# Kernel optimization log

Measured on AMD Instinct MI355X. Metric: run time of the kernel, lower is better.

Reference implementation:

```python
import jax, jax.numpy as jnp
import numpy as np

N, P, C, H, W, M = 2, 3, 80, 64, 64, 524288
HID = 64
BOX_WARP = 2.0


def _linear_init(key, fan_in, fan_out):
    # kaiming-uniform-ish; bias is zero-init per the torch module
    bound = 1.0 / np.sqrt(fan_in)
    return jax.random.uniform(key, (fan_in, fan_out), jnp.float32, -bound, bound)


def setup_inputs() -> dict:
    key = jax.random.key(0)
    ks = jax.random.split(key, 6)
    planes = jax.random.normal(ks[0], (N, P, C, H, W), jnp.float32)
    coordinates = jax.random.uniform(ks[1], (N, M, 3), jnp.float32, -1.0, 1.0)
    W1 = _linear_init(ks[2], 3 * C, HID)
    W2 = _linear_init(ks[3], HID, HID)
    W3 = _linear_init(ks[4], HID, HID)
    W4 = _linear_init(ks[5], HID, 1)
    return {
        "planes": planes, "coordinates": coordinates,
        "W1": W1, "b1": jnp.zeros((HID,), jnp.float32),
        "W2": W2, "b2": jnp.zeros((HID,), jnp.float32),
        "W3": W3, "b3": jnp.zeros((HID,), jnp.float32),
        "W4": W4, "b4": jnp.zeros((1,), jnp.float32),
    }


def _grid_sample_bilinear(feat, grid):
    # feat: [B, C, H, W]; grid: [B, M, 2] in [-1, 1] (x, y order),
    # bilinear, padding_mode='zeros', align_corners=False (matches torch).
    B, Cc, Hh, Ww = feat.shape
    gx = (grid[..., 0] + 1.0) * (Ww * 0.5) - 0.5  # [B, M]
    gy = (grid[..., 1] + 1.0) * (Hh * 0.5) - 0.5
    x0 = jnp.floor(gx)
    y0 = jnp.floor(gy)
    wx1 = gx - x0
    wy1 = gy - y0
    featf = feat.transpose(0, 2, 3, 1).reshape(B, Hh * Ww, Cc)  # [B, HW, C]

    def gather(xi, yi):
        valid = (xi >= 0) & (xi < Ww) & (yi >= 0) & (yi < Hh)
        xc = jnp.clip(xi, 0, Ww - 1).astype(jnp.int32)
        yc = jnp.clip(yi, 0, Hh - 1).astype(jnp.int32)
        idx = yc * Ww + xc  # [B, M]
        v = jnp.take_along_axis(featf, idx[..., None], axis=1)  # [B, M, C]
        return v * valid[..., None].astype(feat.dtype)

    v00 = gather(x0, y0)
    v01 = gather(x0 + 1, y0)
    v10 = gather(x0, y0 + 1)
    v11 = gather(x0 + 1, y0 + 1)
    wx1 = wx1[..., None]
    wy1 = wy1[..., None]
    top = v00 * (1.0 - wx1) + v01 * wx1
    bot = v10 * (1.0 - wx1) + v11 * wx1
    return top * (1.0 - wy1) + bot * wy1  # [B, M, C]


def _plane_axes():
    return jnp.array(
        [[[1, 0, 0], [0, 1, 0], [0, 0, 1]],
         [[1, 0, 0], [0, 0, 1], [0, 1, 0]],
         [[0, 0, 1], [0, 1, 0], [1, 0, 0]]], jnp.float32)


def reference(planes, coordinates, W1, b1, W2, b2, W3, b3, W4, b4):
    n, p, c, h, w = planes.shape
    m = coordinates.shape[1]
    inv_axes = jnp.linalg.inv(_plane_axes())  # [3, 3, 3]
    coords = (2.0 / BOX_WARP) * coordinates  # [N, M, 3]
    # project: coords @ inv_plane per plane, keep first two coords
    proj = jnp.einsum('nmc,pcd->npmd', coords, inv_axes)[..., :2]  # [N, P, M, 2]
    feat = planes.reshape(n * p, c, h, w)
    grid = proj.reshape(n * p, m, 2)
    samp = _grid_sample_bilinear(feat, grid)  # [N*P, M, C]
    # [N, P, M, C] -> [N, M, P*C]
    x = samp.reshape(n, p, m, c).transpose(0, 2, 1, 3).reshape(n, m, p * c)
    hdn = jax.nn.relu(x @ W1 + b1)
    hdn = jax.nn.relu(hdn @ W2 + b2)
    hdn = jax.nn.relu(hdn @ W3 + b3)
    sdf = hdn @ W4 + b4  # [N, M, 1]
    return sdf
```

## Files before the change

### kernel.cpp

```cpp
#include <hip/hip_runtime.h>
#include <hip/hip_bf16.h>
#include <stdint.h>

#define MPTS  524288
#define NB    2
#define CCH   80
#define HWDIM 64
#define HID   64
#define NPTS  (NB * MPTS)

typedef _Float16 f16x2 __attribute__((ext_vector_type(2)));
typedef _Float16 f16x8 __attribute__((ext_vector_type(8)));
typedef float    f32x4 __attribute__((ext_vector_type(4)));

union FragH { uint4 q; f16x8 v; f16x2 h2[4]; _Float16 h[8]; };

__device__ __forceinline__ void fma_mix_lo(float& acc, unsigned u, float w) {
    asm volatile("v_fma_mix_f32 %0, %1, %2, %0 op_sel_hi:[1,0,0]"
                 : "+v"(acc) : "v"(u), "v"(w));
}
__device__ __forceinline__ void fma_mix_hi(float& acc, unsigned u, float w) {
    asm volatile("v_fma_mix_f32 %0, %1, %2, %0 op_sel:[1,0,0] op_sel_hi:[1,0,0]"
                 : "+v"(acc) : "v"(u), "v"(w));
}

__global__ void precompute_planesW(const float* __restrict__ planes,
                                   const float* __restrict__ W1,
                                   unsigned short* __restrict__ planesW) {
    __shared__ float tA[CCH * 64];
    __shared__ float tW[CCH * 64];
    int b  = blockIdx.x;
    int np = b >> 6, y = b & 63;
    int p  = np % 3;
    int t  = threadIdx.x;
    for (int i = t; i < CCH * 64; i += 256) {
        int c = i >> 6, x = i & 63;
        tA[i] = planes[((size_t)np * CCH + c) * 4096 + y * 64 + x];
        tW[i] = W1[(p * CCH + c) * HID + x];
    }
    __syncthreads();
    int px = t >> 2;
    int n0 = (t & 3) * 16;
    float acc[16];
    #pragma unroll
    for (int i = 0; i < 16; ++i) acc[i] = 0.0f;
    for (int c = 0; c < CCH; ++c) {
        float a = tA[c * 64 + px];
        #pragma unroll
        for (int i = 0; i < 16; ++i) acc[i] += a * tW[c * 64 + n0 + i];
    }
    unsigned short* dst = planesW + (((size_t)np * 4096) + y * 64 + px) * HID + n0;
    #pragma unroll
    for (int i = 0; i < 16; ++i) {
        union { _Float16 h; unsigned short u; } cv;
        cv.h = (_Float16)acc[i];
        dst[i] = cv.u;
    }
}

__global__ void pack_weights23(const float* __restrict__ W2,
                               const float* __restrict__ W3,
                               unsigned short* __restrict__ wpack) {
    int e = blockIdx.x * 256 + threadIdx.x;
    const float* W = (e < 4096) ? W2 : W3;
    int q  = e & 4095;
    int j  = q & 7;
    int l  = (q >> 3) & 63;
    int nt = (q >> 9) & 3;
    int kb = q >> 11;
    int k  = kb * 32 + ((l >> 4) << 3) + j;
    int nn = nt * 16 + (l & 15);
    union { _Float16 h; unsigned short u; } cv;
    cv.h = (_Float16)W[k * HID + nn];
    wpack[e] = cv.u;
}

__global__ __launch_bounds__(256, 4) void fused_kernel(
        const unsigned short* __restrict__ planesW,
        const float* __restrict__ coords,
        const unsigned short* __restrict__ wpack,
        const float* __restrict__ b1, const float* __restrict__ b2,
        const float* __restrict__ b3, const float* __restrict__ W4,
        const float* __restrict__ b4, float* __restrict__ out) {

    __shared__ __align__(16) unsigned short sH[4 * 16 * 72];
    __shared__ __align__(16) uint4 sSet[64][3][2];
    __shared__ __align__(16) unsigned short sW23[8192];
    __shared__ float sBias[196];

    int t    = threadIdx.x;
    int wave = t >> 6, lane = t & 63;
    int ptbase = blockIdx.x * 64 + wave * 16;

    unsigned short* hw = sH + wave * (16 * 72);
    _Float16* hwh = (_Float16*)hw;

    {
        const uint4* g = (const uint4*)wpack;
        uint4* s = (uint4*)sW23;
        s[t]       = g[t];
        s[t + 256] = g[t + 256];
        s[t + 512] = g[t + 512];
        s[t + 768] = g[t + 768];
        if (t < 64)        sBias[t] = b2[t];
        else if (t < 128)  sBias[t] = b3[t - 64];
        else if (t < 192)  sBias[t] = W4[t - 128];
        else if (t == 192) sBias[192] = b4[0];
    }

    if (t < 192) {
        int i  = t & 63;
        int p  = t >> 6;
        int mypt = blockIdx.x * 64 + i;
        int n    = mypt >> 19;
        const float* cp = coords + (size_t)mypt * 3;
        float c0 = cp[0], c1 = cp[1], c2 = cp[2];
        float gx = (p == 2) ? c2 : c0;
        float gy = (p == 1) ? c2 : c1;
        float fx = (gx + 1.0f) * 32.0f - 0.5f;
        float fy = (gy + 1.0f) * 32.0f - 0.5f;
        float xf = floorf(fx), yf = floorf(fy);
        float wx = fx - xf,    wy = fy - yf;
        int x0 = (int)xf, y0 = (int)yf, x1 = x0 + 1, y1 = y0 + 1;
        float vx0 = (x0 >= 0 && x0 < 64) ? 1.0f : 0.0f;
        float vx1 = (x1 >= 0 && x1 < 64) ? 1.0f : 0.0f;
        float vy0 = (y0 >= 0 && y0 < 64) ? 1.0f : 0.0f;
        float vy1 = (y1 >= 0 && y1 < 64) ? 1.0f : 0.0f;
        int cx0 = min(max(x0, 0), 63), cx1 = min(max(x1, 0), 63);
        int cy0 = min(max(y0, 0), 63), cy1 = min(max(y1, 0), 63);
        union { float f[4]; uint4 q; } wq;
        wq.f[0] = (1.0f - wx) * (1.0f - wy) * vx0 * vy0;
        wq.f[1] = wx * (1.0f - wy) * vx1 * vy0;
        wq.f[2] = (1.0f - wx) * wy * vx0 * vy1;
        wq.f[3] = wx * wy * vx1 * vy1;
        int base = (n * 3 + p) * 4096;
        uint4 oq;
        oq.x = (unsigned)((base + (cy0 << 6) + cx0) * HID);
        oq.y = (unsigned)((base + (cy0 << 6) + cx1) * HID);
        oq.z = (unsigned)((base + (cy1 << 6) + cx0) * HID);
        oq.w = (unsigned)((base + (cy1 << 6) + cx1) * HID);
        sSet[i][p][0] = oq;
        sSet[i][p][1] = wq.q;
    }
    __syncthreads();

    {
        int sub = lane & 7;
        int ptg = lane >> 3;

        float b1f0, b1f1, b1f2, b1f3, b1f4, b1f5, b1f6, b1f7;
        {
            const float4* bp = (const float4*)(b1 + sub * 8);
            float4 v0 = bp[0], v1 = bp[1];
            b1f0 = v0.x; b1f1 = v0.y; b1f2 = v0.z; b1f3 = v0.w;
            b1f4 = v1.x; b1f5 = v1.y; b1f6 = v1.z; b1f7 = v1.w;
        }
        const unsigned short* pw = planesW + sub * 8;

        auto do_round = [&](int pt) {
            int pl = wave * 16 + pt;
            uint4 o0 = sSet[pl][0][0], w0c = sSet[pl][0][1];
            uint4 o1 = sSet[pl][1][0], w1c = sSet[pl][1][1];
            uint4 o2 = sSet[pl][2][0], w2c = sSet[pl][2][1];

            FragH u0, u1, u2, u3, u4, u5, u6, u7, u8, u9, u10, u11;
            u0.q  = *(const uint4*)(pw + o0.x);
            u1.q  = *(const uint4*)(pw + o0.y);
            u2.q  = *(const uint4*)(pw + o0.z);
            u3.q  = *(const uint4*)(pw + o0.w);
            u4.q  = *(const uint4*)(pw + o1.x);
            u5.q  = *(const uint4*)(pw + o1.y);
            u6.q  = *(const uint4*)(pw + o1.z);
            u7.q  = *(const uint4*)(pw + o1.w);
            u8.q  = *(const uint4*)(pw + o2.x);
            u9.q  = *(const uint4*)(pw + o2.y);
            u10.q = *(const uint4*)(pw + o2.z);
            u11.q = *(const uint4*)(pw + o2.w);

            float a0 = b1f0, a1 = b1f1, a2 = b1f2, a3 = b1f3;
            float a4 = b1f4, a5 = b1f5, a6 = b1f6, a7 = b1f7;
            union { unsigned u; float f; } cvu;

            #define TEXEL(T, WB) { cvu.u = (WB); float w = cvu.f;            \
                fma_mix_lo(a0, T.q.x, w); fma_mix_hi(a1, T.q.x, w);          \
                fma_mix_lo(a2, T.q.y, w); fma_mix_hi(a3, T.q.y, w);          \
                fma_mix_lo(a4, T.q.z, w); fma_mix_hi(a5, T.q.z, w);          \
                fma_mix_lo(a6, T.q.w, w); fma_mix_hi(a7, T.q.w, w); }
            TEXEL(u0,  w0c.x) TEXEL(u1,  w0c.y) TEXEL(u2,  w0c.z) TEXEL(u3,  w0c.w)
            TEXEL(u4,  w1c.x) TEXEL(u5,  w1c.y) TEXEL(u6,  w1c.z) TEXEL(u7,  w1c.w)
            TEXEL(u8,  w2c.x) TEXEL(u9,  w2c.y) TEXEL(u10, w2c.z) TEXEL(u11, w2c.w)
            #undef TEXEL

            FragH hv;
            hv.h[0] = (_Float16)fmaxf(a0, 0.0f);
            hv.h[1] = (_Float16)fmaxf(a1, 0.0f);
            hv.h[2] = (_Float16)fmaxf(a2, 0.0f);
            hv.h[3] = (_Float16)fmaxf(a3, 0.0f);
            hv.h[4] = (_Float16)fmaxf(a4, 0.0f);
            hv.h[5] = (_Float16)fmaxf(a5, 0.0f);
            hv.h[6] = (_Float16)fmaxf(a6, 0.0f);
            hv.h[7] = (_Float16)fmaxf(a7, 0.0f);
            *(uint4*)(hwh + pt * 72 + sub * 8) = hv.q;
        };
        do_round(ptg);
        do_round(8 + ptg);
    }
    __syncthreads();

    int row  = lane & 15;
    int kgrp = lane >> 4;
    f32x4 acc2[4] = {{0,0,0,0},{0,0,0,0},{0,0,0,0},{0,0,0,0}};
    #pragma unroll
    for (int kk = 0; kk < 2; ++kk) {
        FragH au;
        au.q = *(const uint4*)(hw + row * 72 + kk * 32 + kgrp * 8);
        #pragma unroll
        for (int nt = 0; nt < 4; ++nt) {
            FragH bu;
            bu.q = *(const uint4*)(sW23 + (kk * 4 + nt) * 512 + lane * 8);
            acc2[nt] = __builtin_amdgcn_mfma_f32_16x16x32_f16(au.v, bu.v, acc2[nt], 0, 0, 0);
        }
    }
    __syncthreads();

    #pragma unroll
    for (int nt = 0; nt < 4; ++nt) {
        float bb = sBias[nt * 16 + row];
        #pragma unroll
        for (int r = 0; r < 4; ++r) {
            float h = fmaxf(acc2[nt][r] + bb, 0.0f);
            hwh[(kgrp * 4 + r) * 72 + nt * 16 + row] = (_Float16)h;
        }
    }
    __syncthreads();

    f32x4 acc3[4] = {{0,0,0,0},{0,0,0,0},{0,0,0,0},{0,0,0,0}};
    #pragma unroll
    for (int kk = 0; kk < 2; ++kk) {
        FragH au;
        au.q = *(const uint4*)(hw + row * 72 + kk * 32 + kgrp * 8);
        #pragma unroll
        for (int nt = 0; nt < 4; ++nt) {
            FragH bu;
            bu.q = *(const uint4*)(sW23 + 4096 + (kk * 4 + nt) * 512 + lane * 8);
            acc3[nt] = __builtin_amdgcn_mfma_f32_16x16x32_f16(au.v, bu.v, acc3[nt], 0, 0, 0);
        }
    }

    float part[4] = {0.f, 0.f, 0.f, 0.f};
    #pragma unroll
    for (int nt = 0; nt < 4; ++nt) {
        float bb  = sBias[64 + nt * 16 + row];
        float w4v = sBias[128 + nt * 16 + row];
        #pragma unroll
        for (int r = 0; r < 4; ++r) {
            float h = fmaxf(acc3[nt][r] + bb, 0.0f);
            part[r] += h * w4v;
        }
    }
    #pragma unroll
    for (int r = 0; r < 4; ++r) {
        #pragma unroll
        for (int off = 1; off < 16; off <<= 1)
            part[r] += __shfl_xor(part[r], off);
    }
    if (row == 0) {
        float bias4 = sBias[192];
        float4 o;
        o.x = part[0] + bias4; o.y = part[1] + bias4;
        o.z = part[2] + bias4; o.w = part[3] + bias4;
        *(float4*)(out + ptbase + kgrp * 4) = o;
    }
}

extern "C" void kernel_launch(void* const* d_in, const int* in_sizes, int n_in,
                              void* d_out, int out_size, void* d_ws, size_t ws_size,
                              hipStream_t stream) {
    const float* planes = (const float*)d_in[0];
    const float* coords = (const float*)d_in[1];
    const float* W1 = (const float*)d_in[2];
    const float* b1 = (const float*)d_in[3];
    const float* W2 = (const float*)d_in[4];
    const float* b2 = (const float*)d_in[5];
    const float* W3 = (const float*)d_in[6];
    const float* b3 = (const float*)d_in[7];
    const float* W4 = (const float*)d_in[8];
    const float* b4 = (const float*)d_in[9];
    float* out = (float*)d_out;

    unsigned short* planesW = (unsigned short*)d_ws;
    unsigned short* wpack   = (unsigned short*)((char*)d_ws + 3145728);

    hipLaunchKernelGGL(precompute_planesW, dim3(NB * 3 * HWDIM), dim3(256), 0, stream,
                       planes, W1, planesW);
    hipLaunchKernelGGL(pack_weights23, dim3(32), dim3(256), 0, stream,
                       W2, W3, wpack);

    int nblocks = NPTS / 64;
    hipLaunchKernelGGL(fused_kernel, dim3(nblocks), dim3(256), 0, stream,
                       planesW, coords, wpack, b1, b2, b3, W4, b4, out);
}
```

Baseline: 102.0 us.

## Use packed fp16 FMA for bilinear gather-accumulate and drop block barriers

Replaces the per-channel fp32 mixed-precision FMAs in the layer-1 gather accumulation with packed fp16 FMAs on f16x2 pairs. Bilinear weights and bias become duplicated half pairs, and ReLU becomes a packed max. This halves the VALU instruction count for the accumulation, at the cost of accumulating 12 terms in fp16, which loses accuracy. It also removes three __syncthreads around the per-wave LDS hidden buffer. That is safe only if each wave touches just its own hw/hwh region; otherwise it risks races.

```diff
diff --git a/kernel.cpp b/kernel.cpp
--- a/kernel.cpp
+++ b/kernel.cpp
@@ -13,15 +13,16 @@
 typedef _Float16 f16x8 __attribute__((ext_vector_type(8)));
 typedef float    f32x4 __attribute__((ext_vector_type(4)));
 
-union FragH { uint4 q; f16x8 v; f16x2 h2[4]; _Float16 h[8]; };
-
-__device__ __forceinline__ void fma_mix_lo(float& acc, unsigned u, float w) {
-    asm volatile("v_fma_mix_f32 %0, %1, %2, %0 op_sel_hi:[1,0,0]"
-                 : "+v"(acc) : "v"(u), "v"(w));
-}
-__device__ __forceinline__ void fma_mix_hi(float& acc, unsigned u, float w) {
-    asm volatile("v_fma_mix_f32 %0, %1, %2, %0 op_sel:[1,0,0] op_sel_hi:[1,0,0]"
-                 : "+v"(acc) : "v"(u), "v"(w));
+union FragH { uint4 q; f16x8 v; f16x2 h2[4]; unsigned d[4]; _Float16 h[8]; };
+union PkU   { f16x2 v; unsigned u; };
+
+__device__ __forceinline__ void pk_fma(unsigned& acc, unsigned a, unsigned b) {
+    asm volatile("v_pk_fma_f16 %0, %1, %2, %0" : "+v"(acc) : "v"(a), "v"(b));
+}
+__device__ __forceinline__ unsigned pk_relu(unsigned a) {
+    unsigned r;
+    asm volatile("v_pk_max_f16 %0, %1, %2" : "=v"(r) : "v"(a), "v"(0u));
+    return r;
 }
 
 __global__ void precompute_planesW(const float* __restrict__ planes,
@@ -128,11 +129,16 @@
         float vy1 = (y1 >= 0 && y1 < 64) ? 1.0f : 0.0f;
         int cx0 = min(max(x0, 0), 63), cx1 = min(max(x1, 0), 63);
         int cy0 = min(max(y0, 0), 63), cy1 = min(max(y1, 0), 63);
-        union { float f[4]; uint4 q; } wq;
-        wq.f[0] = (1.0f - wx) * (1.0f - wy) * vx0 * vy0;
-        wq.f[1] = wx * (1.0f - wy) * vx1 * vy0;
-        wq.f[2] = (1.0f - wx) * wy * vx0 * vy1;
-        wq.f[3] = wx * wy * vx1 * vy1;
+        float f00 = (1.0f - wx) * (1.0f - wy) * vx0 * vy0;
+        float f01 = wx * (1.0f - wy) * vx1 * vy0;
+        float f10 = (1.0f - wx) * wy * vx0 * vy1;
+        float f11 = wx * wy * vx1 * vy1;
+        uint4 wq;
+        { PkU pk; _Float16 h;
+          h = (_Float16)f00; pk.v = f16x2{h, h}; wq.x = pk.u;
+          h = (_Float16)f01; pk.v = f16x2{h, h}; wq.y = pk.u;
+          h = (_Float16)f10; pk.v = f16x2{h, h}; wq.z = pk.u;
+          h = (_Float16)f11; pk.v = f16x2{h, h}; wq.w = pk.u; }
         int base = (n * 3 + p) * 4096;
         uint4 oq;
         oq.x = (unsigned)((base + (cy0 << 6) + cx0) * HID);
@@ -140,7 +146,7 @@
         oq.z = (unsigned)((base + (cy1 << 6) + cx0) * HID);
         oq.w = (unsigned)((base + (cy1 << 6) + cx1) * HID);
         sSet[i][p][0] = oq;
-        sSet[i][p][1] = wq.q;
+        sSet[i][p][1] = wq;
     }
     __syncthreads();
 
@@ -148,12 +154,15 @@
         int sub = lane & 7;
         int ptg = lane >> 3;
 
-        float b1f0, b1f1, b1f2, b1f3, b1f4, b1f5, b1f6, b1f7;
+        unsigned bp0, bp1, bp2, bp3;
         {
-            const float4* bp = (const float4*)(b1 + sub * 8);
-            float4 v0 = bp[0], v1 = bp[1];
-            b1f0 = v0.x; b1f1 = v0.y; b1f2 = v0.z; b1f3 = v0.w;
-            b1f4 = v1.x; b1f5 = v1.y; b1f6 = v1.z; b1f7 = v1.w;
+            const float4* bpp = (const float4*)(b1 + sub * 8);
+            float4 v0 = bpp[0], v1 = bpp[1];
+            PkU pk;
+            pk.v = f16x2{(_Float16)v0.x, (_Float16)v0.y}; bp0 = pk.u;
+            pk.v = f16x2{(_Float16)v0.z, (_Float16)v0.w}; bp1 = pk.u;
+            pk.v = f16x2{(_Float16)v1.x, (_Float16)v1.y}; bp2 = pk.u;
+            pk.v = f16x2{(_Float16)v1.z, (_Float16)v1.w}; bp3 = pk.u;
         }
         const unsigned short* pw = planesW + sub * 8;
 
@@ -177,35 +186,23 @@
             u10.q = *(const uint4*)(pw + o2.z);
             u11.q = *(const uint4*)(pw + o2.w);
 
-            float a0 = b1f0, a1 = b1f1, a2 = b1f2, a3 = b1f3;
-            float a4 = b1f4, a5 = b1f5, a6 = b1f6, a7 = b1f7;
-            union { unsigned u; float f; } cvu;
-
-            #define TEXEL(T, WB) { cvu.u = (WB); float w = cvu.f;            \
-                fma_mix_lo(a0, T.q.x, w); fma_mix_hi(a1, T.q.x, w);          \
-                fma_mix_lo(a2, T.q.y, w); fma_mix_hi(a3, T.q.y, w);          \
-                fma_mix_lo(a4, T.q.z, w); fma_mix_hi(a5, T.q.z, w);          \
-                fma_mix_lo(a6, T.q.w, w); fma_mix_hi(a7, T.q.w, w); }
+            unsigned a0 = bp0, a1 = bp1, a2 = bp2, a3 = bp3;
+
+            #define TEXEL(T, WB) { pk_fma(a0, T.d[0], WB); pk_fma(a1, T.d[1], WB); \
+                                   pk_fma(a2, T.d[2], WB); pk_fma(a3, T.d[3], WB); }
             TEXEL(u0,  w0c.x) TEXEL(u1,  w0c.y) TEXEL(u2,  w0c.z) TEXEL(u3,  w0c.w)
             TEXEL(u4,  w1c.x) TEXEL(u5,  w1c.y) TEXEL(u6,  w1c.z) TEXEL(u7,  w1c.w)
             TEXEL(u8,  w2c.x) TEXEL(u9,  w2c.y) TEXEL(u10, w2c.z) TEXEL(u11, w2c.w)
             #undef TEXEL
 
-            FragH hv;
-            hv.h[0] = (_Float16)fmaxf(a0, 0.0f);
-            hv.h[1] = (_Float16)fmaxf(a1, 0.0f);
-            hv.h[2] = (_Float16)fmaxf(a2, 0.0f);
-            hv.h[3] = (_Float16)fmaxf(a3, 0.0f);
-            hv.h[4] = (_Float16)fmaxf(a4, 0.0f);
-            hv.h[5] = (_Float16)fmaxf(a5, 0.0f);
-            hv.h[6] = (_Float16)fmaxf(a6, 0.0f);
-            hv.h[7] = (_Float16)fmaxf(a7, 0.0f);
-            *(uint4*)(hwh + pt * 72 + sub * 8) = hv.q;
+            uint4 hv;
+            hv.x = pk_relu(a0); hv.y = pk_relu(a1);
+            hv.z = pk_relu(a2); hv.w = pk_relu(a3);
+            *(uint4*)(hwh + pt * 72 + sub * 8) = hv;
         };
         do_round(ptg);
         do_round(8 + ptg);
     }
-    __syncthreads();
 
     int row  = lane & 15;
     int kgrp = lane >> 4;
@@ -221,7 +218,6 @@
             acc2[nt] = __builtin_amdgcn_mfma_f32_16x16x32_f16(au.v, bu.v, acc2[nt], 0, 0, 0);
         }
     }
-    __syncthreads();
 
     #pragma unroll
     for (int nt = 0; nt < 4; ++nt) {
@@ -232,7 +228,6 @@
             hwh[(kgrp * 4 + r) * 72 + nt * 16 + row] = (_Float16)h;
         }
     }
-    __syncthreads();
 
     f32x4 acc3[4] = {{0,0,0,0},{0,0,0,0},{0,0,0,0},{0,0,0,0}};
     #pragma unroll
```

Result: faster. 96.62 us (-5.2%).
